# Optimization experiments

Hardware: AMD Instinct MI355X
Metric: run time of the kernel (lower is better)

## Reference

```python
import jax, jax.numpy as jnp
import numpy as np

EMBED_DIM = 1024
NUM_HEADS = 16
BATCH = 4
SEQ = 4096


def setup_inputs() -> dict:
    key = jax.random.key(0)
    ks = jax.random.split(key, 5)
    scale = 0.02
    E = EMBED_DIM
    x = jax.random.normal(ks[0], (BATCH, SEQ, E), dtype=jnp.float32)
    Wq = jax.random.normal(ks[1], (E, E), dtype=jnp.float32) * scale
    Wk = jax.random.normal(ks[2], (E, E), dtype=jnp.float32) * scale
    Wv = jax.random.normal(ks[3], (E, E), dtype=jnp.float32) * scale
    Wo = jax.random.normal(ks[4], (E, E), dtype=jnp.float32) * scale
    z = jnp.zeros((E,), dtype=jnp.float32)
    return {"x": x, "Wq": Wq, "bq": z, "Wk": Wk, "bk": z, "Wv": Wv, "bv": z, "Wo": Wo, "bo": z}


def reference(x, Wq, bq, Wk, bk, Wv, bv, Wo, bo):
    B, S, E = x.shape
    H = NUM_HEADS
    D = E // H
    # torch nn.Linear: y = x @ W.T + b
    def proj(W, b):
        return (jnp.einsum('bse,fe->bsf', x, W) + b).reshape(B, S, H, D)
    q = jax.nn.elu(proj(Wq, bq)) + 1.0  # [B,S,H,D] feature map
    k = jax.nn.elu(proj(Wk, bk)) + 1.0
    v = proj(Wv, bv)
    # kv aggregation over sequence: [B,H,D,D]
    kv = jnp.einsum('bshd,bshe->bhde', k, v)
    # Q . KV: [B,S,H,D] -> merge heads -> [B,S,E]
    out = jnp.einsum('bshd,bhde->bshe', q, kv).reshape(B, S, E)
    # output projection (dropout is identity at inference)
    out = jnp.einsum('bse,fe->bsf', out, Wo) + bo
    return out
```

## Files before the change

### kernel.cpp

```cpp
#include <hip/hip_runtime.h>
#include <hip/hip_bf16.h>
#include <cstdint>
#include <cstddef>

#define BATCH 4
#define SEQ   4096
#define EMB   1024
#define M_TOT (BATCH * SEQ)
#define KV_CHUNKS 16

using bf16_t = __hip_bfloat16;
typedef __attribute__((ext_vector_type(8))) short bv8;
typedef __attribute__((ext_vector_type(4))) float f32x4;
typedef __attribute__((ext_vector_type(4))) unsigned short us4;

union SV8 { bv8 v; bf16_t h[8]; };

static __device__ __forceinline__ unsigned short bfbits(float v) {
  bf16_t b = __float2bfloat16(v);
  unsigned short u;
  __builtin_memcpy(&u, &b, 2);
  return u;
}

__device__ __forceinline__ void gload_lds16(const void* g, void* l) {
  __builtin_amdgcn_global_load_lds(
      (const __attribute__((address_space(1))) unsigned int*)g,
      (__attribute__((address_space(3))) unsigned int*)l, 16, 0, 0);
}

#define BAR() asm volatile("s_barrier" ::: "memory")

__global__ __launch_bounds__(256) void cvt_all(
    const float* __restrict__ x, const float* __restrict__ wq,
    const float* __restrict__ wk, const float* __restrict__ wv,
    const float* __restrict__ wo, bf16_t* __restrict__ xb,
    bf16_t* __restrict__ wqkv, bf16_t* __restrict__ wob) {
  const int bid = blockIdx.x;
  const float* in;
  bf16_t* out;
  size_t base;
  if (bid < 8192) {
    in = x; out = xb; base = (size_t)bid * 2048;
  } else {
    const int q = (bid - 8192) >> 9, sub = (bid - 8192) & 511;
    base = (size_t)sub * 2048;
    switch (q) {
      case 0:  in = wq; out = wqkv; break;
      case 1:  in = wk; out = wqkv + 1048576; break;
      case 2:  in = wv; out = wqkv + 2097152; break;
      default: in = wo; out = wob; break;
    }
  }
  const size_t i = base + (size_t)threadIdx.x * 8;
  const f32x4 a = *(const f32x4*)(in + i);
  const f32x4 b = *(const f32x4*)(in + i + 4);
  SV8 o;
#pragma unroll
  for (int j = 0; j < 4; ++j) o.h[j] = __float2bfloat16(a[j]);
#pragma unroll
  for (int j = 0; j < 4; ++j) o.h[4 + j] = __float2bfloat16(b[j]);
  *(bv8*)(out + i) = o.v;
}

template <int VARIANT>
__global__ __launch_bounds__(512, 2) void gemm8p(
    const bf16_t* __restrict__ A, const bf16_t* __restrict__ Wbase,
    const float* __restrict__ b0, const float* __restrict__ b1,
    const float* __restrict__ b2, void* __restrict__ o0,
    void* __restrict__ o1, void* __restrict__ o2) {
  constexpr int K = 1024;
  constexpr int NT = (VARIANT == 0) ? 12 : 4;
  constexpr int NKT = K / 64;
  __shared__ char lds[131072];

  const int nwg = NT * 64;
  const int wg = (blockIdx.x & 7) * (nwg >> 3) + (blockIdx.x >> 3);
  const int m0 = (wg / NT) * 256;
  const int n0 = (wg % NT) * 256;
  const bf16_t* W = Wbase + (VARIANT ? (size_t)(m0 >> 12) * 1048576ull : 0);
  const int t = threadIdx.x, l = t & 63, w = t >> 6;
  const int wm = w >> 2, wn = w & 3;

  const int sr = ((t >> 7) << 4) + (t & 15);
  const int sc = (((t >> 6) & 1) << 5) + (((t >> 4) & 3) << 3);
  const bf16_t* aRow = A + (size_t)(m0 + sr) * K + sc;
  const bf16_t* wRow = W + (size_t)(n0 + sr) * K + sc;
  char* dA = lds + t * 16;
  char* dB = lds + 65536 + t * 16;

  auto ST = [&](int isB, int hf, int kt) {
    char* d = (isB ? dB : dA) + (kt & 1) * 32768 + hf * 16384;
    const bf16_t* s = (isB ? wRow : aRow) + (size_t)(hf * 128) * K + kt * 64;
    gload_lds16(s, d);
    gload_lds16(s + (size_t)64 * K, d + 8192);
  };

  const char* Ab = lds + wm * 16384 + l * 16;
  const char* Bb = lds + 65536 + (wn >> 1) * 16384 + (wn & 1) * 8192 + l * 16;

  f32x4 acc[8][4] = {};
  bv8 af[4][2], bf[4][2];

  ST(1, 0, 0); ST(1, 1, 0); ST(0, 0, 0); ST(0, 1, 0);
  ST(1, 0, 1); ST(1, 1, 1); ST(0, 0, 1);
  asm volatile("s_waitcnt vmcnt(6)" ::: "memory");
  BAR();

#pragma unroll 1
  for (int j = 0; j < NKT; ++j) {
    const int db = (j & 1) * 32768;
#pragma unroll
    for (int mb = 0; mb < 4; ++mb)
#pragma unroll
      for (int ks = 0; ks < 2; ++ks)
        af[mb][ks] = *(const bv8*)(Ab + db + mb * 2048 + ks * 1024);
#pragma unroll
    for (int nb = 0; nb < 4; ++nb)
#pragma unroll
      for (int ks = 0; ks < 2; ++ks)
        bf[nb][ks] = *(const bv8*)(Bb + db + nb * 2048 + ks * 1024);
    if (j + 1 < NKT) ST(0, 1, j + 1);
    BAR();
    __builtin_amdgcn_s_setprio(1);
#pragma unroll
    for (int mb = 0; mb < 4; ++mb)
#pragma unroll
      for (int nb = 0; nb < 2; ++nb)
#pragma unroll
        for (int ks = 0; ks < 2; ++ks)
          acc[mb][nb] = __builtin_amdgcn_mfma_f32_16x16x32_bf16(
              bf[nb][ks], af[mb][ks], acc[mb][nb], 0, 0, 0);
    __builtin_amdgcn_s_setprio(0);
    BAR();
    if (j + 2 < NKT) ST(1, 0, j + 2);
    BAR();
    __builtin_amdgcn_s_setprio(1);
#pragma unroll
    for (int mb = 0; mb < 4; ++mb)
#pragma unroll
      for (int nb = 2; nb < 4; ++nb)
#pragma unroll
        for (int ks = 0; ks < 2; ++ks)
          acc[mb][nb] = __builtin_amdgcn_mfma_f32_16x16x32_bf16(
              bf[nb][ks], af[mb][ks], acc[mb][nb], 0, 0, 0);
    __builtin_amdgcn_s_setprio(0);
    BAR();
#pragma unroll
    for (int mb = 0; mb < 4; ++mb)
#pragma unroll
      for (int ks = 0; ks < 2; ++ks)
        af[mb][ks] = *(const bv8*)(Ab + db + 8192 + mb * 2048 + ks * 1024);
    if (j + 2 < NKT) ST(1, 1, j + 2);
    BAR();
    __builtin_amdgcn_s_setprio(1);
#pragma unroll
    for (int mb = 0; mb < 4; ++mb)
#pragma unroll
      for (int nb = 2; nb < 4; ++nb)
#pragma unroll
        for (int ks = 0; ks < 2; ++ks)
          acc[4 + mb][nb] = __builtin_amdgcn_mfma_f32_16x16x32_bf16(
              bf[nb][ks], af[mb][ks], acc[4 + mb][nb], 0, 0, 0);
    __builtin_amdgcn_s_setprio(0);
    BAR();
    if (j + 2 < NKT) {
      ST(0, 0, j + 2);
      asm volatile("s_waitcnt vmcnt(6)" ::: "memory");
    } else if (j == NKT - 2) {
      asm volatile("s_waitcnt vmcnt(0)" ::: "memory");
    }
    BAR();
    __builtin_amdgcn_s_setprio(1);
#pragma unroll
    for (int mb = 0; mb < 4; ++mb)
#pragma unroll
      for (int nb = 0; nb < 2; ++nb)
#pragma unroll
        for (int ks = 0; ks < 2; ++ks)
          acc[4 + mb][nb] = __builtin_amdgcn_mfma_f32_16x16x32_bf16(
              bf[nb][ks], af[mb][ks], acc[4 + mb][nb], 0, 0, 0);
    __builtin_amdgcn_s_setprio(0);
    BAR();
  }

  const int rl = l & 15;
  const int c4 = (l >> 4) << 2;
  const int rbase = m0 + wm * 128;
  if (VARIANT == 0) {
    const int gq = n0 >> 10;
    const float* bias = gq == 0 ? b0 : (gq == 1 ? b1 : b2);
    bf16_t* ob = (bf16_t*)(gq == 0 ? o0 : (gq == 1 ? o1 : o2));
    const int cb = (n0 & 1023) + wn * 64;
#pragma unroll
    for (int nb = 0; nb < 4; ++nb) {
      const int coln = cb + nb * 16 + c4;
      const f32x4 bz = *(const f32x4*)(bias + coln);
#pragma unroll
      for (int mb = 0; mb < 8; ++mb) {
        us4 pk;
#pragma unroll
        for (int r = 0; r < 4; ++r) {
          float v = acc[mb][nb][r] + bz[r];
          if (gq < 2) v = (v > 0.f) ? (v + 1.f) : __expf(v);
          pk[r] = bfbits(v);
        }
        *(us4*)(ob + (size_t)(rbase + mb * 16 + rl) * 1024 + coln) = pk;
      }
    }
  } else {
    const int cb = n0 + wn * 64;
#pragma unroll
    for (int nb = 0; nb < 4; ++nb) {
      const int coln = cb + nb * 16 + c4;
      const f32x4 bz = *(const f32x4*)(b0 + coln);
#pragma unroll
      for (int mb = 0; mb < 8; ++mb) {
        f32x4 ov;
#pragma unroll
        for (int r = 0; r < 4; ++r) ov[r] = acc[mb][nb][r] + bz[r];
        *(f32x4*)((float*)o0 + (size_t)(rbase + mb * 16 + rl) * 1024 + coln) = ov;
      }
    }
  }
}

__global__ __launch_bounds__(256) void kv_partial(const bf16_t* __restrict__ Kmat,
                                                  const bf16_t* __restrict__ Vmat,
                                                  float* __restrict__ pkv) {
  const int chunk = blockIdx.x;
  const int bh = blockIdx.y;
  const int b = bh >> 4, h = bh & 15;
  const int t = threadIdx.x;
  __shared__ bf16_t kl[8][64], vl[8][64];
  float acc[16] = {};
  const int e = t & 63, d0 = (t >> 6) * 16;
  const int sl = t >> 5, c2 = (t & 31) * 2;
  const int s0 = chunk * (SEQ / KV_CHUNKS);
  const bf16_t* kp = Kmat + ((size_t)(b * SEQ + s0 + sl)) * EMB + h * 64 + c2;
  const bf16_t* vp = Vmat + ((size_t)(b * SEQ + s0 + sl)) * EMB + h * 64 + c2;
  for (int it = 0; it < (SEQ / KV_CHUNKS) / 8; ++it) {
    const unsigned int kw = *(const unsigned int*)kp;
    const unsigned int vw = *(const unsigned int*)vp;
    __syncthreads();
    *(unsigned int*)&kl[sl][c2] = kw;
    *(unsigned int*)&vl[sl][c2] = vw;
    __syncthreads();
#pragma unroll
    for (int ss = 0; ss < 8; ++ss) {
      const float vv = __bfloat162float(vl[ss][e]);
      SV8 k0, k1;
      k0.v = *(const bv8*)&kl[ss][d0];
      k1.v = *(const bv8*)&kl[ss][d0 + 8];
#pragma unroll
      for (int dd = 0; dd < 8; ++dd) acc[dd] += __bfloat162float(k0.h[dd]) * vv;
#pragma unroll
      for (int dd = 0; dd < 8; ++dd) acc[8 + dd] += __bfloat162float(k1.h[dd]) * vv;
    }
    kp += 8 * EMB;
    vp += 8 * EMB;
  }
  float* outp = pkv + ((size_t)chunk * 64 + bh) * 4096;
#pragma unroll
  for (int dd = 0; dd < 16; ++dd) outp[(d0 + dd) * 64 + e] = acc[dd];
}

__global__ __launch_bounds__(256) void fold2(const float* __restrict__ pkv,
                                             const bf16_t* __restrict__ Wo,
                                             bf16_t* __restrict__ MT) {
  __shared__ char lds[24576];
  const int bh = blockIdx.x;
  const int b = bh >> 4, h = bh & 15;
  const int t = threadIdx.x, l = t & 63, w = t >> 6;

  const int d = t >> 2, e0 = (t & 3) * 16;
  float s[16] = {};
#pragma unroll
  for (int c = 0; c < KV_CHUNKS; ++c) {
    const float* pp = pkv + ((size_t)c * 64 + bh) * 4096 + d * 64 + e0;
#pragma unroll
    for (int q = 0; q < 4; ++q) {
      const f32x4 v = *(const f32x4*)(pp + q * 4);
#pragma unroll
      for (int r = 0; r < 4; ++r) s[q * 4 + r] += v[r];
    }
  }
  SV8 p0, p1;
#pragma unroll
  for (int j = 0; j < 8; ++j) p0.h[j] = __float2bfloat16(s[j]);
#pragma unroll
  for (int j = 0; j < 8; ++j) p1.h[j] = __float2bfloat16(s[8 + j]);
  const int fb0 = (d >> 4) * 2048 + (d & 15) * 16;
  *(bv8*)(lds + fb0 + (e0 >> 5) * 1024 + ((e0 >> 3) & 3) * 256) = p0.v;
  const int e1 = e0 + 8;
  *(bv8*)(lds + fb0 + (e1 >> 5) * 1024 + ((e1 >> 3) & 3) * 256) = p1.v;
  __syncthreads();

  bv8 bn[4][2];
#pragma unroll
  for (int db = 0; db < 4; ++db)
#pragma unroll
    for (int ks = 0; ks < 2; ++ks)
      bn[db][ks] = *(const bv8*)(lds + db * 2048 + ks * 1024 + l * 16);

  bf16_t* outB = MT + (size_t)b * 1048576ull + h * 64;
  const int rl = l & 15, c4 = (l >> 4) << 2;
  for (int ft = 0; ft < 8; ++ft) {
#pragma unroll
    for (int q = 0; q < 4; ++q) {
      const int sslot = q * 256 + t;
      const int row = ((sslot >> 7) << 4) + (sslot & 15);
      const int col = (((sslot >> 6) & 1) << 5) + (((sslot >> 4) & 3) << 3);
      gload_lds16(Wo + (size_t)(ft * 128 + row) * 1024 + h * 64 + col,
                  lds + 8192 + sslot * 16);
    }
    asm volatile("s_waitcnt vmcnt(0)" ::: "memory");
    __syncthreads();
    f32x4 acc[4][2] = {};
    bv8 am[2][2];
#pragma unroll
    for (int i = 0; i < 2; ++i)
#pragma unroll
      for (int ks = 0; ks < 2; ++ks)
        am[i][ks] = *(const bv8*)(lds + 8192 + (w * 2 + i) * 2048 + ks * 1024 + l * 16);
#pragma unroll
    for (int db = 0; db < 4; ++db)
#pragma unroll
      for (int i = 0; i < 2; ++i)
#pragma unroll
        for (int ks = 0; ks < 2; ++ks)
          acc[db][i] = __builtin_amdgcn_mfma_f32_16x16x32_bf16(
              bn[db][ks], am[i][ks], acc[db][i], 0, 0, 0);
#pragma unroll
    for (int i = 0; i < 2; ++i)
#pragma unroll
      for (int db = 0; db < 4; ++db) {
        us4 pk;
#pragma unroll
        for (int r = 0; r < 4; ++r) pk[r] = bfbits(acc[db][i][r]);
        const int f = ft * 128 + w * 32 + i * 16 + rl;
        *(us4*)(outB + (size_t)f * 1024 + db * 16 + c4) = pk;
      }
    __syncthreads();
  }
}

extern "C" void kernel_launch(void* const* d_in, const int* in_sizes, int n_in,
                              void* d_out, int out_size, void* d_ws, size_t ws_size,
                              hipStream_t stream) {
  (void)in_sizes; (void)n_in; (void)out_size;
  const float* x  = (const float*)d_in[0];
  const float* Wq = (const float*)d_in[1];
  const float* bq = (const float*)d_in[2];
  const float* Wk = (const float*)d_in[3];
  const float* bk = (const float*)d_in[4];
  const float* Wv = (const float*)d_in[5];
  const float* bv = (const float*)d_in[6];
  const float* Wo = (const float*)d_in[7];
  const float* bo = (const float*)d_in[8];

  const size_t NEED = 72ull * 1024 * 1024;
  if (ws_size < NEED) return;

  char* p = (char*)d_ws;
  bf16_t* xb   = (bf16_t*)p;
  float*  pkv  = (float*)p;
  bf16_t* MT   = (bf16_t*)(p + 17825792ull);
  bf16_t* wqkv = (bf16_t*)(p + 33554432ull);
  bf16_t* wob  = (bf16_t*)(p + 39845888ull);
  bf16_t* qb   = (bf16_t*)(p + 41943040ull);

  bf16_t* kb = (bf16_t*)d_out;
  bf16_t* vb = kb + 16777216ull;

  cvt_all<<<10240, 256, 0, stream>>>(x, Wq, Wk, Wv, Wo, xb, wqkv, wob);

  gemm8p<0><<<768, 512, 0, stream>>>(xb, wqkv, bq, bk, bv, qb, kb, vb);

  kv_partial<<<dim3(KV_CHUNKS, 64), 256, 0, stream>>>(kb, vb, pkv);
  fold2<<<64, 256, 0, stream>>>(pkv, wob, MT);

  gemm8p<1><<<256, 512, 0, stream>>>(qb, MT, bo, nullptr, nullptr,
                                     d_out, nullptr, nullptr);
}
```

Measured before the change: 401.0 us.

## Make QKV GEMM persistent with three tiles per workgroup and cross-tile prefetch

The QKV projection GEMM now launches 256 workgroups, each processing three consecutive 256x256 output tiles, instead of 768 one-tile workgroups. The global-to-LDS prefetch pipeline continues across tile boundaries, so loads for the next tile's first k-steps overlap the current tile's final MFMAs and epilogue. This targets the per-tile pipeline fill/drain cost and the wave-quantization tail. In exchange, the epilogue stores now sit serially inside the loop, and with 256 CUs and 2 WGs per CU occupancy may be only one WG per CU, which reduces latency hiding.

```diff
diff --git a/kernel.cpp b/kernel.cpp
--- a/kernel.cpp
+++ b/kernel.cpp
@@ -63,37 +63,41 @@
   *(bv8*)(out + i) = o.v;
 }
 
-template <int VARIANT>
-__global__ __launch_bounds__(512, 2) void gemm8p(
+template <int VARIANT, int NTILES>
+__device__ __forceinline__ void gemm_body(
     const bf16_t* __restrict__ A, const bf16_t* __restrict__ Wbase,
     const float* __restrict__ b0, const float* __restrict__ b1,
     const float* __restrict__ b2, void* __restrict__ o0,
-    void* __restrict__ o1, void* __restrict__ o2) {
+    void* __restrict__ o1, void* __restrict__ o2, char* lds) {
   constexpr int K = 1024;
   constexpr int NT = (VARIANT == 0) ? 12 : 4;
-  constexpr int NKT = K / 64;
-  __shared__ char lds[131072];
-
-  const int nwg = NT * 64;
+  constexpr int JTOT = NTILES * 16;
+
+  const int nwg = NT * 64 / NTILES;
   const int wg = (blockIdx.x & 7) * (nwg >> 3) + (blockIdx.x >> 3);
-  const int m0 = (wg / NT) * 256;
-  const int n0 = (wg % NT) * 256;
-  const bf16_t* W = Wbase + (VARIANT ? (size_t)(m0 >> 12) * 1048576ull : 0);
   const int t = threadIdx.x, l = t & 63, w = t >> 6;
   const int wm = w >> 2, wn = w & 3;
 
   const int sr = ((t >> 7) << 4) + (t & 15);
   const int sc = (((t >> 6) & 1) << 5) + (((t >> 4) & 3) << 3);
-  const bf16_t* aRow = A + (size_t)(m0 + sr) * K + sc;
-  const bf16_t* wRow = W + (size_t)(n0 + sr) * K + sc;
   char* dA = lds + t * 16;
   char* dB = lds + 65536 + t * 16;
 
-  auto ST = [&](int isB, int hf, int kt) {
-    char* d = (isB ? dB : dA) + (kt & 1) * 32768 + hf * 16384;
-    const bf16_t* s = (isB ? wRow : aRow) + (size_t)(hf * 128) * K + kt * 64;
-    gload_lds16(s, d);
-    gload_lds16(s + (size_t)64 * K, d + 8192);
+  auto ST = [&](int isB, int hf, int gkt) {
+    if (gkt >= JTOT) return;
+    const int tau = (NTILES == 1) ? wg : (NTILES * wg + (gkt >> 4));
+    const int kt = gkt & 15;
+    const int m0s = (tau / NT) * 256, n0s = (tau % NT) * 256;
+    const bf16_t* src;
+    if (isB) {
+      const bf16_t* Wt = Wbase + (VARIANT ? (size_t)(m0s >> 12) * 1048576ull : 0);
+      src = Wt + (size_t)(n0s + hf * 128 + sr) * K + kt * 64 + sc;
+    } else {
+      src = A + (size_t)(m0s + hf * 128 + sr) * K + kt * 64 + sc;
+    }
+    char* d = (isB ? dB : dA) + (gkt & 1) * 32768 + hf * 16384;
+    gload_lds16(src, d);
+    gload_lds16(src + (size_t)64 * K, d + 8192);
   };
 
   const char* Ab = lds + wm * 16384 + l * 16;
@@ -108,121 +112,157 @@
   BAR();
 
 #pragma unroll 1
-  for (int j = 0; j < NKT; ++j) {
-    const int db = (j & 1) * 32768;
-#pragma unroll
-    for (int mb = 0; mb < 4; ++mb)
-#pragma unroll
-      for (int ks = 0; ks < 2; ++ks)
-        af[mb][ks] = *(const bv8*)(Ab + db + mb * 2048 + ks * 1024);
-#pragma unroll
-    for (int nb = 0; nb < 4; ++nb)
-#pragma unroll
-      for (int ks = 0; ks < 2; ++ks)
-        bf[nb][ks] = *(const bv8*)(Bb + db + nb * 2048 + ks * 1024);
-    if (j + 1 < NKT) ST(0, 1, j + 1);
-    BAR();
-    __builtin_amdgcn_s_setprio(1);
-#pragma unroll
-    for (int mb = 0; mb < 4; ++mb)
-#pragma unroll
-      for (int nb = 0; nb < 2; ++nb)
+  for (int tt = 0; tt < NTILES; ++tt) {
+    const int tau_c = (NTILES == 1) ? wg : (NTILES * wg + tt);
+    const int m0 = (tau_c / NT) * 256, n0 = (tau_c % NT) * 256;
+
+#pragma unroll 1
+    for (int j = 0; j < 16; ++j) {
+      const int gj = tt * 16 + j;
+      const int db = (gj & 1) * 32768;
+#pragma unroll
+      for (int mb = 0; mb < 4; ++mb)
 #pragma unroll
         for (int ks = 0; ks < 2; ++ks)
-          acc[mb][nb] = __builtin_amdgcn_mfma_f32_16x16x32_bf16(
-              bf[nb][ks], af[mb][ks], acc[mb][nb], 0, 0, 0);
-    __builtin_amdgcn_s_setprio(0);
-    BAR();
-    if (j + 2 < NKT) ST(1, 0, j + 2);
-    BAR();
-    __builtin_amdgcn_s_setprio(1);
-#pragma unroll
-    for (int mb = 0; mb < 4; ++mb)
-#pragma unroll
-      for (int nb = 2; nb < 4; ++nb)
+          af[mb][ks] = *(const bv8*)(Ab + db + mb * 2048 + ks * 1024);
+#pragma unroll
+      for (int nb = 0; nb < 4; ++nb)
 #pragma unroll
         for (int ks = 0; ks < 2; ++ks)
-          acc[mb][nb] = __builtin_amdgcn_mfma_f32_16x16x32_bf16(
-              bf[nb][ks], af[mb][ks], acc[mb][nb], 0, 0, 0);
-    __builtin_amdgcn_s_setprio(0);
-    BAR();
-#pragma unroll
-    for (int mb = 0; mb < 4; ++mb)
-#pragma unroll
-      for (int ks = 0; ks < 2; ++ks)
-        af[mb][ks] = *(const bv8*)(Ab + db + 8192 + mb * 2048 + ks * 1024);
-    if (j + 2 < NKT) ST(1, 1, j + 2);
-    BAR();
-    __builtin_amdgcn_s_setprio(1);
-#pragma unroll
-    for (int mb = 0; mb < 4; ++mb)
-#pragma unroll
-      for (int nb = 2; nb < 4; ++nb)
+          bf[nb][ks] = *(const bv8*)(Bb + db + nb * 2048 + ks * 1024);
+      ST(0, 1, gj + 1);
+      BAR();
+      __builtin_amdgcn_s_setprio(1);
+#pragma unroll
+      for (int mb = 0; mb < 4; ++mb)
+#pragma unroll
+        for (int nb = 0; nb < 2; ++nb)
+#pragma unroll
+          for (int ks = 0; ks < 2; ++ks)
+            acc[mb][nb] = __builtin_amdgcn_mfma_f32_16x16x32_bf16(
+                bf[nb][ks], af[mb][ks], acc[mb][nb], 0, 0, 0);
+      __builtin_amdgcn_s_setprio(0);
+      BAR();
+      ST(1, 0, gj + 2);
+      BAR();
+      __builtin_amdgcn_s_setprio(1);
+#pragma unroll
+      for (int mb = 0; mb < 4; ++mb)
+#pragma unroll
+        for (int nb = 2; nb < 4; ++nb)
+#pragma unroll
+          for (int ks = 0; ks < 2; ++ks)
+            acc[mb][nb] = __builtin_amdgcn_mfma_f32_16x16x32_bf16(
+                bf[nb][ks], af[mb][ks], acc[mb][nb], 0, 0, 0);
+      __builtin_amdgcn_s_setprio(0);
+      BAR();
+#pragma unroll
+      for (int mb = 0; mb < 4; ++mb)
 #pragma unroll
         for (int ks = 0; ks < 2; ++ks)
-          acc[4 + mb][nb] = __builtin_amdgcn_mfma_f32_16x16x32_bf16(
-              bf[nb][ks], af[mb][ks], acc[4 + mb][nb], 0, 0, 0);
-    __builtin_amdgcn_s_setprio(0);
-    BAR();
-    if (j + 2 < NKT) {
-      ST(0, 0, j + 2);
-      asm volatile("s_waitcnt vmcnt(6)" ::: "memory");
-    } else if (j == NKT - 2) {
-      asm volatile("s_waitcnt vmcnt(0)" ::: "memory");
-    }
-    BAR();
-    __builtin_amdgcn_s_setprio(1);
-#pragma unroll
-    for (int mb = 0; mb < 4; ++mb)
-#pragma unroll
-      for (int nb = 0; nb < 2; ++nb)
-#pragma unroll
-        for (int ks = 0; ks < 2; ++ks)
-          acc[4 + mb][nb] = __builtin_amdgcn_mfma_f32_16x16x32_bf16(
-              bf[nb][ks], af[mb][ks], acc[4 + mb][nb], 0, 0, 0);
-    __builtin_amdgcn_s_setprio(0);
-    BAR();
+          af[mb][ks] = *(const bv8*)(Ab + db + 8192 + mb * 2048 + ks * 1024);
+      ST(1, 1, gj + 2);
+      BAR();
+      __builtin_amdgcn_s_setprio(1);
+#pragma unroll
+      for (int mb = 0; mb < 4; ++mb)
+#pragma unroll
+        for (int nb = 2; nb < 4; ++nb)
+#pragma unroll
+          for (int ks = 0; ks < 2; ++ks)
+            acc[4 + mb][nb] = __builtin_amdgcn_mfma_f32_16x16x32_bf16(
+                bf[nb][ks], af[mb][ks], acc[4 + mb][nb], 0, 0, 0);
+      __builtin_amdgcn_s_setprio(0);
+      BAR();
+      if (gj + 2 < JTOT) {
+        ST(0, 0, gj + 2);
+        asm volatile("s_waitcnt vmcnt(6)" ::: "memory");
+      } else if (gj == JTOT - 2) {
+        asm volatile("s_waitcnt vmcnt(0)" ::: "memory");
+      }
+      BAR();
+      __builtin_amdgcn_s_setprio(1);
+#pragma unroll
+      for (int mb = 0; mb < 4; ++mb)
+#pragma unroll
+        for (int nb = 0; nb < 2; ++nb)
+#pragma unroll
+          for (int ks = 0; ks < 2; ++ks)
+            acc[4 + mb][nb] = __builtin_amdgcn_mfma_f32_16x16x32_bf16(
+                bf[nb][ks], af[mb][ks], acc[4 + mb][nb], 0, 0, 0);
+      __builtin_amdgcn_s_setprio(0);
+      BAR();
+    }
+
+    {
+      const int rl = l & 15;
+      const int c4 = (l >> 4) << 2;
+      const int rbase = m0 + wm * 128;
+      if (VARIANT == 0) {
+        const int gq = n0 >> 10;
+        const float* bias = gq == 0 ? b0 : (gq == 1 ? b1 : b2);
+        bf16_t* ob = (bf16_t*)(gq == 0 ? o0 : (gq == 1 ? o1 : o2));
+        const int cb = (n0 & 1023) + wn * 64;
+        f32x4 bz[4];
+#pragma unroll
+        for (int nb = 0; nb < 4; ++nb) bz[nb] = *(const f32x4*)(bias + cb + nb * 16 + c4);
+#pragma unroll
+        for (int mb = 0; mb < 8; ++mb) {
+          const size_t rowoff = (size_t)(rbase + mb * 16 + rl) * 1024;
+#pragma unroll
+          for (int nb = 0; nb < 4; ++nb) {
+            us4 pk;
+#pragma unroll
+            for (int r = 0; r < 4; ++r) {
+              float v = acc[mb][nb][r] + bz[nb][r];
+              if (gq < 2) v = (v > 0.f) ? (v + 1.f) : __expf(v);
+              pk[r] = bfbits(v);
+            }
+            *(us4*)(ob + rowoff + cb + nb * 16 + c4) = pk;
+          }
+        }
+      } else {
+        const int cb = n0 + wn * 64;
+        f32x4 bz[4];
+#pragma unroll
+        for (int nb = 0; nb < 4; ++nb) bz[nb] = *(const f32x4*)(b0 + cb + nb * 16 + c4);
+#pragma unroll
+        for (int mb = 0; mb < 8; ++mb) {
+          const size_t rowoff = (size_t)(rbase + mb * 16 + rl) * 1024;
+#pragma unroll
+          for (int nb = 0; nb < 4; ++nb) {
+            f32x4 ov;
+#pragma unroll
+            for (int r = 0; r < 4; ++r) ov[r] = acc[mb][nb][r] + bz[nb][r];
+            *(f32x4*)((float*)o0 + rowoff + cb + nb * 16 + c4) = ov;
+          }
+        }
+      }
+      if (tt + 1 < NTILES) {
+#pragma unroll
+        for (int mb = 0; mb < 8; ++mb)
+#pragma unroll
+          for (int nb = 0; nb < 4; ++nb)
+#pragma unroll
+            for (int r = 0; r < 4; ++r) acc[mb][nb][r] = 0.f;
+      }
+    }
   }
-
-  const int rl = l & 15;
-  const int c4 = (l >> 4) << 2;
-  const int rbase = m0 + wm * 128;
-  if (VARIANT == 0) {
-    const int gq = n0 >> 10;
-    const float* bias = gq == 0 ? b0 : (gq == 1 ? b1 : b2);
-    bf16_t* ob = (bf16_t*)(gq == 0 ? o0 : (gq == 1 ? o1 : o2));
-    const int cb = (n0 & 1023) + wn * 64;
-#pragma unroll
-    for (int nb = 0; nb < 4; ++nb) {
-      const int coln = cb + nb * 16 + c4;
-      const f32x4 bz = *(const f32x4*)(bias + coln);
-#pragma unroll
-      for (int mb = 0; mb < 8; ++mb) {
-        us4 pk;
-#pragma unroll
-        for (int r = 0; r < 4; ++r) {
-          float v = acc[mb][nb][r] + bz[r];
-          if (gq < 2) v = (v > 0.f) ? (v + 1.f) : __expf(v);
-          pk[r] = bfbits(v);
-        }
-        *(us4*)(ob + (size_t)(rbase + mb * 16 + rl) * 1024 + coln) = pk;
-      }
-    }
-  } else {
-    const int cb = n0 + wn * 64;
-#pragma unroll
-    for (int nb = 0; nb < 4; ++nb) {
-      const int coln = cb + nb * 16 + c4;
-      const f32x4 bz = *(const f32x4*)(b0 + coln);
-#pragma unroll
-      for (int mb = 0; mb < 8; ++mb) {
-        f32x4 ov;
-#pragma unroll
-        for (int r = 0; r < 4; ++r) ov[r] = acc[mb][nb][r] + bz[r];
-        *(f32x4*)((float*)o0 + (size_t)(rbase + mb * 16 + rl) * 1024 + coln) = ov;
-      }
-    }
-  }
+}
+
+__global__ __launch_bounds__(512, 2) void gqkv_k(
+    const bf16_t* __restrict__ A, const bf16_t* __restrict__ W,
+    const float* __restrict__ b0, const float* __restrict__ b1,
+    const float* __restrict__ b2, void* o0, void* o1, void* o2) {
+  __shared__ char lds[131072];
+  gemm_body<0, 3>(A, W, b0, b1, b2, o0, o1, o2, lds);
+}
+
+__global__ __launch_bounds__(512, 2) void gout_k(
+    const bf16_t* __restrict__ A, const bf16_t* __restrict__ W,
+    const float* __restrict__ b0, void* o0) {
+  __shared__ char lds[131072];
+  gemm_body<1, 1>(A, W, b0, nullptr, nullptr, o0, nullptr, nullptr, lds);
 }
 
 __global__ __launch_bounds__(256) void kv_partial(const bf16_t* __restrict__ Kmat,
@@ -375,11 +415,10 @@
 
   cvt_all<<<10240, 256, 0, stream>>>(x, Wq, Wk, Wv, Wo, xb, wqkv, wob);
 
-  gemm8p<0><<<768, 512, 0, stream>>>(xb, wqkv, bq, bk, bv, qb, kb, vb);
+  gqkv_k<<<256, 512, 0, stream>>>(xb, wqkv, bq, bk, bv, qb, kb, vb);
 
   kv_partial<<<dim3(KV_CHUNKS, 64), 256, 0, stream>>>(kb, vb, pkv);
   fold2<<<64, 256, 0, stream>>>(pkv, wob, MT);
 
-  gemm8p<1><<<256, 512, 0, stream>>>(qb, MT, bo, nullptr, nullptr,
-                                     d_out, nullptr, nullptr);
-}
+  gout_k<<<256, 512, 0, stream>>>(qb, MT, bo, d_out);
+}
```

Measured after the change: 372.3 us. 1.08x faster.
